# Kernel optimization log

Measured on AMD Instinct MI355X. Metric: run time of the kernel, lower is better.

## Reference

```python
import jax, jax.numpy as jnp
import numpy as np

HID = 512
POOL = 4096
N_OBJ = 1280
N_REL = 16384
NUM_OBJ_CLS = 151
NUM_REL_CLS = 51


def setup_inputs() -> dict:
    key = jax.random.key(0)
    ks = jax.random.split(key, 12)
    return {
        'edge_ctx': jax.random.normal(ks[0], (N_OBJ, HID), dtype=jnp.float32),
        'union_features': jax.random.normal(ks[1], (N_REL, POOL), dtype=jnp.float32),
        'W_post_emb': jax.random.normal(ks[2], (HID, 2 * HID), dtype=jnp.float32) * (10.0 / np.sqrt(HID)),
        'b_post_emb': jax.random.normal(ks[3], (2 * HID,), dtype=jnp.float32) * 0.01,
        'W_post_cat': jax.random.normal(ks[4], (2 * HID, POOL), dtype=jnp.float32) * 0.02,
        'b_post_cat': jnp.zeros((POOL,), dtype=jnp.float32),
        'W_rel': jax.random.normal(ks[5], (POOL, NUM_REL_CLS), dtype=jnp.float32) * 0.02,
        'b_rel': jnp.zeros((NUM_REL_CLS,), dtype=jnp.float32),
        'freq_table': jax.random.normal(ks[6], (NUM_OBJ_CLS * NUM_OBJ_CLS, NUM_REL_CLS), dtype=jnp.float32),
        'pair_idx': jax.random.randint(ks[7], (N_REL, 2), 0, N_OBJ, dtype=jnp.int32),
        'obj_preds': jax.random.randint(ks[8], (N_OBJ,), 0, NUM_OBJ_CLS, dtype=jnp.int32),
    }


def reference(edge_ctx, union_features, W_post_emb, b_post_emb, W_post_cat,
              b_post_cat, W_rel, b_rel, freq_table, pair_idx, obj_preds):
    # post_emb: [N_obj, 2*hid]; view(N,2,hid) -> head = first hid, tail = last hid
    edge_rep = edge_ctx @ W_post_emb + b_post_emb
    head_rep = edge_rep[:, :HID]   # [N_obj, hid]
    tail_rep = edge_rep[:, HID:]   # [N_obj, hid]

    # gather subject/object reps per relation pair, concat -> [N_rel, 2*hid]
    prod_rep = jnp.concatenate(
        (head_rep[pair_idx[:, 0]], tail_rep[pair_idx[:, 1]]), axis=-1)

    prod_rep = prod_rep @ W_post_cat + b_post_cat        # [N_rel, pool]
    prod_rep = prod_rep * union_features                  # use_vision fuse
    rel_dists = prod_rep @ W_rel + b_rel                  # [N_rel, num_rel]

    # frequency bias: Embedding over [num_obj^2, num_rel] indexed by label pair
    bias_idx = obj_preds[pair_idx[:, 0]] * NUM_OBJ_CLS + obj_preds[pair_idx[:, 1]]
    rel_dists = rel_dists + freq_table[bias_idx]
    return rel_dists
```

## Files before the change

kernel.cpp:

```cpp
#include <hip/hip_runtime.h>

#define HID 512
#define POOL 4096
#define N_OBJ 1280
#define N_REL 16384
#define NOC 151
#define NRC 51

typedef _Float16 half_t;
typedef half_t h16x8 __attribute__((ext_vector_type(8)));
typedef float f32x4 __attribute__((ext_vector_type(4)));

#define LDSTR 72

__global__ __launch_bounds__(256) void k1_edge_rep(
    const float* __restrict__ edge_ctx,
    const float* __restrict__ We,
    const float* __restrict__ be,
    half_t* __restrict__ E)
{
    __shared__ __align__(16) half_t As[64 * LDSTR];
    __shared__ __align__(16) half_t Bs[64 * LDSTR];

    const int m0 = blockIdx.x * 64;
    const int n0 = blockIdx.y * 64;
    const int t = threadIdx.x;
    const int wave = t >> 6, lane = t & 63;
    const int quad = lane >> 4, l16 = lane & 15;

    const int ar  = t >> 2;
    const int akb = (t & 3) * 16;
    const int bn  = (t & 15) * 4;
    const int bk  = t >> 4;

    f32x4 acc[4] = {};

    for (int k0 = 0; k0 < HID; k0 += 64) {
        {
            const float* src = edge_ctx + (m0 + ar) * HID + k0 + akb;
#pragma unroll
            for (int i = 0; i < 2; ++i) {
                float4 va = *(const float4*)(src + 8 * i);
                float4 vb = *(const float4*)(src + 8 * i + 4);
                h16x8 o;
                o[0] = (half_t)va.x; o[1] = (half_t)va.y;
                o[2] = (half_t)va.z; o[3] = (half_t)va.w;
                o[4] = (half_t)vb.x; o[5] = (half_t)vb.y;
                o[6] = (half_t)vb.z; o[7] = (half_t)vb.w;
                *(h16x8*)&As[ar * LDSTR + akb + 8 * i] = o;
            }
        }
#pragma unroll
        for (int it = 0; it < 4; ++it) {
            int kk = bk + 16 * it;
            float4 v = *(const float4*)(We + (size_t)(k0 + kk) * 1024 + n0 + bn);
            Bs[(bn + 0) * LDSTR + kk] = (half_t)v.x;
            Bs[(bn + 1) * LDSTR + kk] = (half_t)v.y;
            Bs[(bn + 2) * LDSTR + kk] = (half_t)v.z;
            Bs[(bn + 3) * LDSTR + kk] = (half_t)v.w;
        }
        __syncthreads();
#pragma unroll
        for (int s = 0; s < 2; ++s) {
            h16x8 a = *(const h16x8*)&As[(wave * 16 + l16) * LDSTR + s * 32 + quad * 8];
#pragma unroll
            for (int nt = 0; nt < 4; ++nt) {
                h16x8 b = *(const h16x8*)&Bs[(nt * 16 + l16) * LDSTR + s * 32 + quad * 8];
                acc[nt] = __builtin_amdgcn_mfma_f32_16x16x32_f16(a, b, acc[nt], 0, 0, 0);
            }
        }
        __syncthreads();
    }
#pragma unroll
    for (int nt = 0; nt < 4; ++nt) {
        int n = n0 + nt * 16 + l16;
        float bias = be[n];
#pragma unroll
        for (int r = 0; r < 4; ++r) {
            int m = m0 + wave * 16 + quad * 4 + r;
            E[(size_t)m * 1024 + n] = (half_t)(acc[nt][r] + bias);
        }
    }
}

__global__ __launch_bounds__(256) void k2_ht(
    const half_t* __restrict__ E,
    const float* __restrict__ Wc,
    const float* __restrict__ bcat,
    half_t* __restrict__ Hws,
    half_t* __restrict__ Tws)
{
    __shared__ __align__(16) half_t As[64 * LDSTR];
    __shared__ __align__(16) half_t Bs[64 * LDSTR];

    const int z  = blockIdx.z;
    const int m0 = blockIdx.x * 64;
    const int n0 = blockIdx.y * 64;
    const int t = threadIdx.x;
    const int wave = t >> 6, lane = t & 63;
    const int quad = lane >> 4, l16 = lane & 15;

    const int ar  = t >> 2;
    const int akb = (t & 3) * 16;
    const int bn  = (t & 15) * 4;
    const int bk  = t >> 4;

    f32x4 acc[4] = {};

    for (int k0 = 0; k0 < HID; k0 += 64) {
        {
            const half_t* src = E + (size_t)(m0 + ar) * 1024 + z * 512 + k0 + akb;
            *(h16x8*)&As[ar * LDSTR + akb]     = *(const h16x8*)(src);
            *(h16x8*)&As[ar * LDSTR + akb + 8] = *(const h16x8*)(src + 8);
        }
#pragma unroll
        for (int it = 0; it < 4; ++it) {
            int kk = bk + 16 * it;
            float4 v = *(const float4*)(Wc + (size_t)(z * 512 + k0 + kk) * POOL + n0 + bn);
            Bs[(bn + 0) * LDSTR + kk] = (half_t)v.x;
            Bs[(bn + 1) * LDSTR + kk] = (half_t)v.y;
            Bs[(bn + 2) * LDSTR + kk] = (half_t)v.z;
            Bs[(bn + 3) * LDSTR + kk] = (half_t)v.w;
        }
        __syncthreads();
#pragma unroll
        for (int s = 0; s < 2; ++s) {
            h16x8 a = *(const h16x8*)&As[(wave * 16 + l16) * LDSTR + s * 32 + quad * 8];
#pragma unroll
            for (int nt = 0; nt < 4; ++nt) {
                h16x8 b = *(const h16x8*)&Bs[(nt * 16 + l16) * LDSTR + s * 32 + quad * 8];
                acc[nt] = __builtin_amdgcn_mfma_f32_16x16x32_f16(a, b, acc[nt], 0, 0, 0);
            }
        }
        __syncthreads();
    }
    half_t* outp = z ? Tws : Hws;
#pragma unroll
    for (int nt = 0; nt < 4; ++nt) {
        int n = n0 + nt * 16 + l16;
        float bias = z ? 0.0f : bcat[n];
#pragma unroll
        for (int r = 0; r < 4; ++r) {
            int m = m0 + wave * 16 + quad * 4 + r;
            outp[(size_t)m * POOL + n] = (half_t)(acc[nt][r] + bias);
        }
    }
}

__global__ __launch_bounds__(256) void k2b_wt(
    const float* __restrict__ Wrel, half_t* __restrict__ Wt)
{
    int k = blockIdx.x * 256 + threadIdx.x;
#pragma unroll 8
    for (int n = 0; n < 64; ++n) {
        float v = (n < NRC) ? Wrel[(size_t)k * NRC + n] : 0.0f;
        Wt[(size_t)n * POOL + k] = (half_t)v;
    }
}

__global__ __launch_bounds__(256) void k3_main(
    const float* __restrict__ unionf,
    const half_t* __restrict__ Hws,
    const half_t* __restrict__ Tws,
    const half_t* __restrict__ Wt,
    const float* __restrict__ brel,
    const float* __restrict__ freq,
    const int* __restrict__ pair_idx,
    const int* __restrict__ obj_preds,
    float* __restrict__ out)
{
    __shared__ __align__(16) half_t As[64 * LDSTR];
    __shared__ __align__(16) half_t Bs[64 * LDSTR];

    const int R0 = blockIdx.x * 64;
    const int t = threadIdx.x;
    const int wave = t >> 6, lane = t & 63;
    const int quad = lane >> 4, l16 = lane & 15;

    const int ar  = t >> 2;
    const int akb = (t & 3) * 16;

    const int2 pr = *(const int2*)(pair_idx + 2 * (R0 + ar));
    const half_t* Hrow = Hws + (size_t)pr.x * POOL;
    const half_t* Trow = Tws + (size_t)pr.y * POOL;
    const float*  urow = unionf + (size_t)(R0 + ar) * POOL;

    f32x4 acc[4] = {};

    for (int k0 = 0; k0 < POOL; k0 += 64) {
#pragma unroll
        for (int i = 0; i < 2; ++i) {
            h16x8 hv = *(const h16x8*)(Hrow + k0 + akb + 8 * i);
            h16x8 tv = *(const h16x8*)(Trow + k0 + akb + 8 * i);
            float4 ua = *(const float4*)(urow + k0 + akb + 8 * i);
            float4 ub = *(const float4*)(urow + k0 + akb + 8 * i + 4);
            h16x8 o;
            o[0] = (half_t)(((float)hv[0] + (float)tv[0]) * ua.x);
            o[1] = (half_t)(((float)hv[1] + (float)tv[1]) * ua.y);
            o[2] = (half_t)(((float)hv[2] + (float)tv[2]) * ua.z);
            o[3] = (half_t)(((float)hv[3] + (float)tv[3]) * ua.w);
            o[4] = (half_t)(((float)hv[4] + (float)tv[4]) * ub.x);
            o[5] = (half_t)(((float)hv[5] + (float)tv[5]) * ub.y);
            o[6] = (half_t)(((float)hv[6] + (float)tv[6]) * ub.z);
            o[7] = (half_t)(((float)hv[7] + (float)tv[7]) * ub.w);
            *(h16x8*)&As[ar * LDSTR + akb + 8 * i] = o;
        }
        {
            const half_t* src = Wt + (size_t)ar * POOL + k0 + akb;
            *(h16x8*)&Bs[ar * LDSTR + akb]     = *(const h16x8*)(src);
            *(h16x8*)&Bs[ar * LDSTR + akb + 8] = *(const h16x8*)(src + 8);
        }
        __syncthreads();
#pragma unroll
        for (int s = 0; s < 2; ++s) {
            h16x8 a = *(const h16x8*)&As[(wave * 16 + l16) * LDSTR + s * 32 + quad * 8];
#pragma unroll
            for (int nt = 0; nt < 4; ++nt) {
                h16x8 b = *(const h16x8*)&Bs[(nt * 16 + l16) * LDSTR + s * 32 + quad * 8];
                acc[nt] = __builtin_amdgcn_mfma_f32_16x16x32_f16(a, b, acc[nt], 0, 0, 0);
            }
        }
        __syncthreads();
    }
#pragma unroll
    for (int r = 0; r < 4; ++r) {
        int grow = R0 + wave * 16 + quad * 4 + r;
        int2 p = *(const int2*)(pair_idx + 2 * grow);
        int fidx = obj_preds[p.x] * NOC + obj_preds[p.y];
        const float* frow = freq + (size_t)fidx * NRC;
#pragma unroll
        for (int nt = 0; nt < 4; ++nt) {
            int n = nt * 16 + l16;
            if (n < NRC)
                out[(size_t)grow * NRC + n] = acc[nt][r] + brel[n] + frow[n];
        }
    }
}

extern "C" void kernel_launch(void* const* d_in, const int* in_sizes, int n_in,
                              void* d_out, int out_size, void* d_ws, size_t ws_size,
                              hipStream_t stream) {
    const float* edge_ctx  = (const float*)d_in[0];
    const float* unionf    = (const float*)d_in[1];
    const float* We        = (const float*)d_in[2];
    const float* be        = (const float*)d_in[3];
    const float* Wc        = (const float*)d_in[4];
    const float* bcat      = (const float*)d_in[5];
    const float* Wrel      = (const float*)d_in[6];
    const float* brel      = (const float*)d_in[7];
    const float* freq      = (const float*)d_in[8];
    const int*   pair_idx  = (const int*)d_in[9];
    const int*   obj_preds = (const int*)d_in[10];
    float* out = (float*)d_out;

    char* ws = (char*)d_ws;
    half_t* E  = (half_t*)(ws);
    half_t* H  = (half_t*)(ws + 2621440);
    half_t* T  = (half_t*)(ws + 13107200);
    half_t* Wt = (half_t*)(ws + 23592960);

    k1_edge_rep<<<dim3(N_OBJ / 64, 1024 / 64), 256, 0, stream>>>(edge_ctx, We, be, E);
    k2b_wt<<<POOL / 256, 256, 0, stream>>>(Wrel, Wt);
    k2_ht<<<dim3(N_OBJ / 64, POOL / 64, 2), 256, 0, stream>>>(E, Wc, bcat, H, T);
    k3_main<<<N_REL / 64, 256, 0, stream>>>(unionf, H, T, Wt, brel, freq,
                                            pair_idx, obj_preds, out);
}
```

Before: 514.4 us.

## Split-K the main relation GEMM with atomics and pre-transpose weights to fp16

The main kernel now splits the 4096-long reduction across four blocks per row tile, which quadruples the grid from 256 blocks so more CUs have work. Partial sums are combined with atomicAdd into an output that is zeroed with a memset first. Separately, W_post_emb and W_post_cat are transposed and converted to fp16 once by a new transpose kernel, so k1 and k2 can load B tiles with vector loads instead of scalar strided LDS stores. The cost is extra launches, a memset, more workspace, and non-deterministic float atomics.

```diff
diff --git a/kernel.cpp b/kernel.cpp
--- a/kernel.cpp
+++ b/kernel.cpp
@@ -6,6 +6,7 @@
 #define N_REL 16384
 #define NOC 151
 #define NRC 51
+#define KSPLIT 4
 
 typedef _Float16 half_t;
 typedef half_t h16x8 __attribute__((ext_vector_type(8)));
@@ -13,9 +14,32 @@
 
 #define LDSTR 72
 
+__global__ __launch_bounds__(256) void kt_transpose(
+    const float* __restrict__ src, half_t* __restrict__ dst, int K, int N)
+{
+    __shared__ __align__(16) half_t Ts[64 * LDSTR];
+    const int kb = blockIdx.x * 64, nb = blockIdx.y * 64;
+    const int t = threadIdx.x;
+    const int kr = t >> 4;
+    const int nc = (t & 15) * 4;
+#pragma unroll
+    for (int p = 0; p < 4; ++p) {
+        float4 v = *(const float4*)(src + (size_t)(kb + kr + 16 * p) * N + nb + nc);
+        Ts[(nc + 0) * LDSTR + kr + 16 * p] = (half_t)v.x;
+        Ts[(nc + 1) * LDSTR + kr + 16 * p] = (half_t)v.y;
+        Ts[(nc + 2) * LDSTR + kr + 16 * p] = (half_t)v.z;
+        Ts[(nc + 3) * LDSTR + kr + 16 * p] = (half_t)v.w;
+    }
+    __syncthreads();
+    const int n = t >> 2, kk = (t & 3) * 16;
+    half_t* d = dst + (size_t)(nb + n) * K + kb + kk;
+    *(h16x8*)(d)     = *(const h16x8*)&Ts[n * LDSTR + kk];
+    *(h16x8*)(d + 8) = *(const h16x8*)&Ts[n * LDSTR + kk + 8];
+}
+
 __global__ __launch_bounds__(256) void k1_edge_rep(
     const float* __restrict__ edge_ctx,
-    const float* __restrict__ We,
+    const half_t* __restrict__ Wet,
     const float* __restrict__ be,
     half_t* __restrict__ E)
 {
@@ -30,14 +54,12 @@
 
     const int ar  = t >> 2;
     const int akb = (t & 3) * 16;
-    const int bn  = (t & 15) * 4;
-    const int bk  = t >> 4;
 
     f32x4 acc[4] = {};
 
     for (int k0 = 0; k0 < HID; k0 += 64) {
         {
-            const float* src = edge_ctx + (m0 + ar) * HID + k0 + akb;
+            const float* src = edge_ctx + (size_t)(m0 + ar) * HID + k0 + akb;
 #pragma unroll
             for (int i = 0; i < 2; ++i) {
                 float4 va = *(const float4*)(src + 8 * i);
@@ -50,14 +72,10 @@
                 *(h16x8*)&As[ar * LDSTR + akb + 8 * i] = o;
             }
         }
-#pragma unroll
-        for (int it = 0; it < 4; ++it) {
-            int kk = bk + 16 * it;
-            float4 v = *(const float4*)(We + (size_t)(k0 + kk) * 1024 + n0 + bn);
-            Bs[(bn + 0) * LDSTR + kk] = (half_t)v.x;
-            Bs[(bn + 1) * LDSTR + kk] = (half_t)v.y;
-            Bs[(bn + 2) * LDSTR + kk] = (half_t)v.z;
-            Bs[(bn + 3) * LDSTR + kk] = (half_t)v.w;
+        {
+            const half_t* src = Wet + (size_t)(n0 + ar) * HID + k0 + akb;
+            *(h16x8*)&Bs[ar * LDSTR + akb]     = *(const h16x8*)(src);
+            *(h16x8*)&Bs[ar * LDSTR + akb + 8] = *(const h16x8*)(src + 8);
         }
         __syncthreads();
 #pragma unroll
@@ -85,7 +103,7 @@
 
 __global__ __launch_bounds__(256) void k2_ht(
     const half_t* __restrict__ E,
-    const float* __restrict__ Wc,
+    const half_t* __restrict__ Wct,
     const float* __restrict__ bcat,
     half_t* __restrict__ Hws,
     half_t* __restrict__ Tws)
@@ -102,8 +120,6 @@
 
     const int ar  = t >> 2;
     const int akb = (t & 3) * 16;
-    const int bn  = (t & 15) * 4;
-    const int bk  = t >> 4;
 
     f32x4 acc[4] = {};
 
@@ -113,14 +129,10 @@
             *(h16x8*)&As[ar * LDSTR + akb]     = *(const h16x8*)(src);
             *(h16x8*)&As[ar * LDSTR + akb + 8] = *(const h16x8*)(src + 8);
         }
-#pragma unroll
-        for (int it = 0; it < 4; ++it) {
-            int kk = bk + 16 * it;
-            float4 v = *(const float4*)(Wc + (size_t)(z * 512 + k0 + kk) * POOL + n0 + bn);
-            Bs[(bn + 0) * LDSTR + kk] = (half_t)v.x;
-            Bs[(bn + 1) * LDSTR + kk] = (half_t)v.y;
-            Bs[(bn + 2) * LDSTR + kk] = (half_t)v.z;
-            Bs[(bn + 3) * LDSTR + kk] = (half_t)v.w;
+        {
+            const half_t* src = Wct + (size_t)(n0 + ar) * 1024 + z * 512 + k0 + akb;
+            *(h16x8*)&Bs[ar * LDSTR + akb]     = *(const h16x8*)(src);
+            *(h16x8*)&Bs[ar * LDSTR + akb + 8] = *(const h16x8*)(src + 8);
         }
         __syncthreads();
 #pragma unroll
@@ -173,6 +185,7 @@
     __shared__ __align__(16) half_t Bs[64 * LDSTR];
 
     const int R0 = blockIdx.x * 64;
+    const int kbase = blockIdx.y * (POOL / KSPLIT);
     const int t = threadIdx.x;
     const int wave = t >> 6, lane = t & 63;
     const int quad = lane >> 4, l16 = lane & 15;
@@ -187,7 +200,7 @@
 
     f32x4 acc[4] = {};
 
-    for (int k0 = 0; k0 < POOL; k0 += 64) {
+    for (int k0 = kbase; k0 < kbase + POOL / KSPLIT; k0 += 64) {
 #pragma unroll
         for (int i = 0; i < 2; ++i) {
             h16x8 hv = *(const h16x8*)(Hrow + k0 + akb + 8 * i);
@@ -222,17 +235,23 @@
         }
         __syncthreads();
     }
+    const bool first = (blockIdx.y == 0);
 #pragma unroll
     for (int r = 0; r < 4; ++r) {
         int grow = R0 + wave * 16 + quad * 4 + r;
-        int2 p = *(const int2*)(pair_idx + 2 * grow);
-        int fidx = obj_preds[p.x] * NOC + obj_preds[p.y];
-        const float* frow = freq + (size_t)fidx * NRC;
+        const float* frow = nullptr;
+        if (first) {
+            int2 p = *(const int2*)(pair_idx + 2 * grow);
+            frow = freq + (size_t)(obj_preds[p.x] * NOC + obj_preds[p.y]) * NRC;
+        }
 #pragma unroll
         for (int nt = 0; nt < 4; ++nt) {
             int n = nt * 16 + l16;
-            if (n < NRC)
-                out[(size_t)grow * NRC + n] = acc[nt][r] + brel[n] + frow[n];
+            if (n < NRC) {
+                float v = acc[nt][r];
+                if (first) v += brel[n] + frow[n];
+                atomicAdd(&out[(size_t)grow * NRC + n], v);
+            }
         }
     }
 }
@@ -254,14 +273,20 @@
     float* out = (float*)d_out;
 
     char* ws = (char*)d_ws;
-    half_t* E  = (half_t*)(ws);
-    half_t* H  = (half_t*)(ws + 2621440);
-    half_t* T  = (half_t*)(ws + 13107200);
-    half_t* Wt = (half_t*)(ws + 23592960);
-
-    k1_edge_rep<<<dim3(N_OBJ / 64, 1024 / 64), 256, 0, stream>>>(edge_ctx, We, be, E);
+    half_t* E   = (half_t*)(ws);
+    half_t* H   = (half_t*)(ws + 2621440);
+    half_t* T   = (half_t*)(ws + 13107200);
+    half_t* Wt  = (half_t*)(ws + 23592960);
+    half_t* Wct = (half_t*)(ws + 24117248);
+    half_t* Wet = (half_t*)(ws + 32505856);
+
+    hipMemsetAsync(out, 0, (size_t)out_size * sizeof(float), stream);
+
+    kt_transpose<<<dim3(HID / 64, 1024 / 64), 256, 0, stream>>>(We, Wet, HID, 1024);
+    kt_transpose<<<dim3(1024 / 64, POOL / 64), 256, 0, stream>>>(Wc, Wct, 1024, POOL);
     k2b_wt<<<POOL / 256, 256, 0, stream>>>(Wrel, Wt);
-    k2_ht<<<dim3(N_OBJ / 64, POOL / 64, 2), 256, 0, stream>>>(E, Wc, bcat, H, T);
-    k3_main<<<N_REL / 64, 256, 0, stream>>>(unionf, H, T, Wt, brel, freq,
-                                            pair_idx, obj_preds, out);
-}
+    k1_edge_rep<<<dim3(N_OBJ / 64, 1024 / 64), 256, 0, stream>>>(edge_ctx, Wet, be, E);
+    k2_ht<<<dim3(N_OBJ / 64, POOL / 64, 2), 256, 0, stream>>>(E, Wct, bcat, H, T);
+    k3_main<<<dim3(N_REL / 64, KSPLIT), 256, 0, stream>>>(unionf, H, T, Wt, brel, freq,
+                                                          pair_idx, obj_preds, out);
+}
```

Measured after the change: 478.5 us. 7.0% less time.
